# Optimization experiments

Hardware: AMD Instinct MI355X
Metric: run time of the kernel (lower is better)

Reference implementation:

```python
import jax, jax.numpy as jnp
import numpy as np

N_TOKENS = 16384
DIM = 2048
HIDDEN = 1408
N_EXPERTS = 8


def setup_inputs() -> dict:
    key = jax.random.key(0)
    k_x, k_w1, k_w2, k_w3 = jax.random.split(key, 4)
    x = jax.random.normal(k_x, (N_TOKENS, DIM), dtype=jnp.float32)
    # trunc_normal(std=0.02) approximated by scaled normal
    w1 = jax.random.normal(k_w1, (N_EXPERTS, HIDDEN, DIM), dtype=jnp.float32) * 0.02
    w2 = jax.random.normal(k_w2, (N_EXPERTS, DIM, HIDDEN), dtype=jnp.float32) * 0.02
    w3 = jax.random.normal(k_w3, (N_EXPERTS, HIDDEN, DIM), dtype=jnp.float32) * 0.02
    # contiguous, even token split across experts (sums to N_TOKENS)
    num_tokens_per_expert = jnp.full((N_EXPERTS,), N_TOKENS // N_EXPERTS, dtype=jnp.int32)
    return {"x": x, "w1": w1, "w2": w2, "w3": w3,
            "num_tokens_per_expert": num_tokens_per_expert}


def reference(x, w1, w2, w3, num_tokens_per_expert):
    """Masked per-expert SwiGLU FFN (matches _run_experts_for_loop).

    x: [N, D] tokens sorted so expert e owns the contiguous slice
       [cumsum_shifted[e], cumsum[e]).
    """
    n_tokens = x.shape[0]
    n_experts = w1.shape[0]
    cumsum = jnp.cumsum(num_tokens_per_expert.astype(jnp.int32))
    cumsum_shifted = jnp.concatenate(
        [jnp.zeros((1,), dtype=cumsum.dtype), cumsum[:-1]])
    token_idx = jnp.arange(n_tokens)
    out = jnp.zeros_like(x)
    for e in range(n_experts):  # small fixed expert loop, unrolled under jit
        mask = ((token_idx >= cumsum_shifted[e]) & (token_idx < cumsum[e]))
        mask = mask.astype(x.dtype)[:, None]          # [N, 1]
        x_masked = x * mask                            # [N, D]
        h = jax.nn.silu(x_masked @ w1[e].T)            # [N, H]
        h = h * (x_masked @ w3[e].T)                   # [N, H]
        out = out + (h @ w2[e].T) * mask               # [N, D]
    return out
```

## Files before the change

### kernel.cpp

```cpp
#include <hip/hip_runtime.h>
#include <stdint.h>

#define NTOK 16384
#define DIM 2048
#define HIDDEN 1408
#define NEXP 8
#define NPRIME 2816

typedef short short8 __attribute__((ext_vector_type(8)));
typedef float f32x4 __attribute__((ext_vector_type(4)));
typedef unsigned short u16;

__device__ __forceinline__ u16 f2bf(float f) {
    uint32_t u = __float_as_uint(f);
    return (u16)((u + 0x7fffu + ((u >> 16) & 1u)) >> 16);
}

__device__ __forceinline__ void gload16(const u16* g, u16* l) {
    __builtin_amdgcn_global_load_lds(
        (const __attribute__((address_space(1))) void*)g,
        (__attribute__((address_space(3))) void*)l,
        16, 0, 0);
}

__device__ __forceinline__ void stageA(const u16* Ag, size_t lda, int k2, u16* dst, int tid) {
    #pragma unroll
    for (int it = 0; it < 4; ++it) {
        int c   = it * 512 + tid;
        int row = c >> 3;
        int sc  = ((c & 7) ^ (row & 7)) << 3;
        gload16(Ag + (size_t)row * lda + k2 + sc, dst + c * 16 / 2);
    }
}
__device__ __forceinline__ void stageB(const u16* Bg, size_t ldb, int k2, u16* dst, int tid) {
    #pragma unroll
    for (int it = 0; it < 2; ++it) {
        int c   = it * 512 + tid;
        int row = c >> 3;
        int sc  = ((c & 7) ^ (row & 7)) << 3;
        gload16(Bg + (size_t)row * ldb + k2 + sc, dst + c * 8);
    }
}

__global__ __launch_bounds__(256) void cvt_kernel(const float* __restrict__ src,
                                                  u16* __restrict__ dst, long n) {
    long i0 = ((long)blockIdx.x * 256 + threadIdx.x) * 8;
    long stride = (long)gridDim.x * 256 * 8;
    for (long i = i0; i < n; i += stride) {
        float4 a = *(const float4*)(src + i);
        float4 b = *(const float4*)(src + i + 4);
        uint4 o;
        o.x = (uint32_t)f2bf(a.x) | ((uint32_t)f2bf(a.y) << 16);
        o.y = (uint32_t)f2bf(a.z) | ((uint32_t)f2bf(a.w) << 16);
        o.z = (uint32_t)f2bf(b.x) | ((uint32_t)f2bf(b.y) << 16);
        o.w = (uint32_t)f2bf(b.z) | ((uint32_t)f2bf(b.w) << 16);
        *(uint4*)(dst + i) = o;
    }
}

__global__ __launch_bounds__(256) void cvt13_kernel(const float* __restrict__ w1,
                                                    const float* __restrict__ w3,
                                                    u16* __restrict__ dst) {
    const int r  = blockIdx.x;
    const int e  = r / NPRIME;
    const int np = r - e * NPRIME;
    const int p  = np >> 5;
    const int s  = (np >> 4) & 1;
    const int c  = np & 15;
    const int hcol = p * 16 + c;
    const float* src = (s ? w3 : w1) + ((size_t)e * HIDDEN + hcol) * DIM;
    u16* d = dst + (size_t)r * DIM;
    const int i = threadIdx.x * 8;
    float4 a = *(const float4*)(src + i);
    float4 b = *(const float4*)(src + i + 4);
    uint4 o;
    o.x = (uint32_t)f2bf(a.x) | ((uint32_t)f2bf(a.y) << 16);
    o.y = (uint32_t)f2bf(a.z) | ((uint32_t)f2bf(a.w) << 16);
    o.z = (uint32_t)f2bf(b.x) | ((uint32_t)f2bf(b.y) << 16);
    o.w = (uint32_t)f2bf(b.z) | ((uint32_t)f2bf(b.w) << 16);
    *(uint4*)(d + i) = o;
}


#define GEMM_CORE(LD, NT, ACC_DECL)                                              \
    const int tid  = threadIdx.x;                                                \
    const int lane = tid & 63;                                                   \
    const int wid  = tid >> 6;                                                   \
    const int wr   = wid >> 1;                         \
    const int wc   = wid & 1;                          \
    const int lq   = lane >> 4;                                                  \
    const int lm   = lane & 15;                                                  \
    ACC_DECL;                                                                    \
    stageA(Ag, LD, 0,  As[0], tid);  stageB(Bg, LD, 0,  Bs[0], tid);             \
    stageA(Ag, LD, 64, As[1], tid);  stageB(Bg, LD, 64, Bs[1], tid);             \
    asm volatile("s_waitcnt vmcnt(6)" ::: "memory");                             \
    __builtin_amdgcn_s_barrier();                                                \
    for (int t = 0; t < NT; ++t) {                                               \
        const int p = t % 3, q = (t + 2) % 3;                                    \
        const u16* Asp = As[p];                                                  \
        const u16* Bsp = Bs[p];                                                  \
        short8 af0[2][2], af1[2][2], bf[4][2];                                   \
        _Pragma("unroll")                                                        \
        for (int i = 0; i < 2; ++i)                                              \
            _Pragma("unroll")                                                    \
            for (int kk = 0; kk < 2; ++kk) {                                     \
                int ar = wr * 64 + i * 16 + lm;                                  \
                int gc = kk * 4 + lq;                                            \
                af0[i][kk] = *(const short8*)&Asp[ar * 64 + ((gc ^ (ar & 7)) << 3)]; \
            }                                                                    \
        _Pragma("unroll")                                                        \
        for (int j = 0; j < 4; ++j)                                              \
            _Pragma("unroll")                                                    \
            for (int kk = 0; kk < 2; ++kk) {                                     \
                int br = wc * 64 + j * 16 + lm;                                  \
                int gc = kk * 4 + lq;                                            \
                bf[j][kk] = *(const short8*)&Bsp[br * 64 + ((gc ^ (br & 7)) << 3)]; \
            }                                                                    \
        if (t + 2 < NT) stageA(Ag, LD, (t + 2) * 64, As[q], tid);                \
        __builtin_amdgcn_s_barrier();                                            \
        __builtin_amdgcn_s_setprio(1);                                           \
        _Pragma("unroll")                                                        \
        for (int kk = 0; kk < 2; ++kk)                                           \
            _Pragma("unroll")                                                    \
            for (int i = 0; i < 2; ++i)                                          \
                _Pragma("unroll")                                                \
                for (int j = 0; j < 4; ++j)                                      \
                    acc[i][j] = __builtin_amdgcn_mfma_f32_16x16x32_bf16(         \
                        af0[i][kk], bf[j][kk], acc[i][j], 0, 0, 0);              \
        __builtin_amdgcn_s_setprio(0);                                           \
        __builtin_amdgcn_s_barrier();                                            \
        _Pragma("unroll")                                                        \
        for (int i = 0; i < 2; ++i)                                              \
            _Pragma("unroll")                                                    \
            for (int kk = 0; kk < 2; ++kk) {                                     \
                int ar = wr * 64 + (i + 2) * 16 + lm;                            \
                int gc = kk * 4 + lq;                                            \
                af1[i][kk] = *(const short8*)&Asp[ar * 64 + ((gc ^ (ar & 7)) << 3)]; \
            }                                                                    \
        if (t + 2 < NT) stageB(Bg, LD, (t + 2) * 64, Bs[q], tid);                \
        __builtin_amdgcn_s_barrier();                                            \
        __builtin_amdgcn_s_setprio(1);                                           \
        _Pragma("unroll")                                                        \
        for (int kk = 0; kk < 2; ++kk)                                           \
            _Pragma("unroll")                                                    \
            for (int i = 0; i < 2; ++i)                                          \
                _Pragma("unroll")                                                \
                for (int j = 0; j < 4; ++j)                                      \
                    acc[i + 2][j] = __builtin_amdgcn_mfma_f32_16x16x32_bf16(     \
                        af1[i][kk], bf[j][kk], acc[i + 2][j], 0, 0, 0);          \
        __builtin_amdgcn_s_setprio(0);                                           \
        if (t + 2 < NT) { asm volatile("s_waitcnt vmcnt(6)" ::: "memory"); }     \
        else            { asm volatile("s_waitcnt vmcnt(0)" ::: "memory"); }     \
        __builtin_amdgcn_s_barrier();                                            \
    }

__global__ __launch_bounds__(512, 1) void ffn1_kernel(
    const u16* __restrict__ xb, const u16* __restrict__ wb13,
    const int* __restrict__ ntpe, u16* __restrict__ hb)
{
    __shared__ u16 As[3][256 * 64];
    __shared__ u16 Bs[3][128 * 64];

    const int nwg = 8 * 22 * NEXP;
    int logical = (blockIdx.x & 7) * (nwg >> 3) + (blockIdx.x >> 3);
    const int mt = logical & 7;
    int rest = logical >> 3;
    const int nt = rest % 22;
    const int e  = rest / 22;

    int base = 0;
    #pragma unroll
    for (int i = 0; i < NEXP; ++i) base += (i < e) ? ntpe[i] : 0;
    const int cnt = ntpe[e];
    if (mt * 256 >= cnt) return;

    const size_t m0 = (size_t)base + (size_t)mt * 256;
    const u16* Ag = xb   + m0 * DIM;
    const u16* Bg = wb13 + ((size_t)e * NPRIME + nt * 128) * DIM;

    GEMM_CORE(DIM, 32, f32x4 acc[4][4] = {})

    #pragma unroll
    for (int i = 0; i < 4; ++i)
        #pragma unroll
        for (int jp = 0; jp < 4; jp += 2) {
            const int p = nt * 4 + wc * 2 + (jp >> 1);
            #pragma unroll
            for (int r = 0; r < 4; ++r) {
                int mrow = mt * 256 + wr * 64 + i * 16 + lq * 4 + r;
                if (mrow < cnt) {
                    float v1 = acc[i][jp][r];
                    float v3 = acc[i][jp + 1][r];
                    float h = (v1 / (1.f + __expf(-v1))) * v3;
                    hb[((size_t)base + mrow) * HIDDEN + p * 16 + lm] = f2bf(h);
                }
            }
        }
}

__global__ __launch_bounds__(512, 1) void ffn2_kernel(
    const u16* __restrict__ hb, const u16* __restrict__ w2b,
    const int* __restrict__ ntpe, float* __restrict__ out)
{
    __shared__ u16 As[3][256 * 64];
    __shared__ u16 Bs[3][128 * 64];

    const int nwg = 8 * 16 * NEXP;
    int logical = (blockIdx.x & 7) * (nwg >> 3) + (blockIdx.x >> 3);
    const int mt = logical & 7;
    int rest = logical >> 3;
    const int nt = rest % 16;
    const int e  = rest / 16;

    int base = 0;
    #pragma unroll
    for (int i = 0; i < NEXP; ++i) base += (i < e) ? ntpe[i] : 0;
    const int cnt = ntpe[e];
    if (mt * 256 >= cnt) return;

    const size_t m0 = (size_t)base + (size_t)mt * 256;
    const u16* Ag = hb  + m0 * HIDDEN;
    const u16* Bg = w2b + ((size_t)e * DIM + nt * 128) * HIDDEN;

    GEMM_CORE(HIDDEN, 22, f32x4 acc[4][4] = {})

    #pragma unroll
    for (int i = 0; i < 4; ++i)
        #pragma unroll
        for (int j = 0; j < 4; ++j)
            #pragma unroll
            for (int r = 0; r < 4; ++r) {
                int mrow = mt * 256 + wr * 64 + i * 16 + lq * 4 + r;
                if (mrow < cnt)
                    out[((size_t)base + mrow) * DIM + (nt * 128 + wc * 64 + j * 16 + lm)] = acc[i][j][r];
            }
}

extern "C" void kernel_launch(void* const* d_in, const int* in_sizes, int n_in,
                              void* d_out, int out_size, void* d_ws, size_t ws_size,
                              hipStream_t stream) {
    const float* x  = (const float*)d_in[0];
    const float* w1 = (const float*)d_in[1];
    const float* w2 = (const float*)d_in[2];
    const float* w3 = (const float*)d_in[3];
    const int* ntpe = (const int*)d_in[4];
    float* out = (float*)d_out;

    u16* xb   = (u16*)d_ws;
    u16* wb13 = xb   + (size_t)NTOK * DIM;
    u16* w2b  = wb13 + (size_t)NEXP * NPRIME * DIM;
    u16* hb   = w2b  + (size_t)NEXP * DIM * HIDDEN;

    cvt_kernel<<<2048, 256, 0, stream>>>(x,  xb,  (long)NTOK * DIM);
    cvt_kernel<<<2048, 256, 0, stream>>>(w2, w2b, (long)NEXP * DIM * HIDDEN);
    cvt13_kernel<<<NEXP * NPRIME, 256, 0, stream>>>(w1, w3, wb13);

    ffn1_kernel<<<8 * 22 * NEXP, 512, 0, stream>>>(xb, wb13, ntpe, hb);
    ffn2_kernel<<<8 * 16 * NEXP, 512, 0, stream>>>(hb, w2b, ntpe, out);
}
```

Baseline: 508.6 us.

## Enlarge GEMM tiles to 256x256 with two-stage half-tile staging

Both FFN GEMMs move from 256x128 output tiles with a three-stage LDS ring to 256x256 tiles with a double-buffered LDS layout. Each K-step is split into four phases, and each phase issues loads for one half of the next A or B tile. The wave grid becomes 2x4 with 8x4 accumulators per wave, which roughly halves the workgroup count and raises operand reuse per LDS load. The costs are a larger register footprint, a shallower prefetch pipeline and coarser tail waves, and the launch bounds now request two blocks per CU.

```diff
diff --git a/kernel.cpp b/kernel.cpp
--- a/kernel.cpp
+++ b/kernel.cpp
@@ -23,22 +23,26 @@
         16, 0, 0);
 }
 
-__device__ __forceinline__ void stageA(const u16* Ag, size_t lda, int k2, u16* dst, int tid) {
-    #pragma unroll
-    for (int it = 0; it < 4; ++it) {
-        int c   = it * 512 + tid;
-        int row = c >> 3;
-        int sc  = ((c & 7) ^ (row & 7)) << 3;
-        gload16(Ag + (size_t)row * lda + k2 + sc, dst + c * 16 / 2);
-    }
-}
-__device__ __forceinline__ void stageB(const u16* Bg, size_t ldb, int k2, u16* dst, int tid) {
+__device__ __forceinline__ void stage_half_A(const u16* Ag, size_t ld, int k2,
+                                             int h, u16* Abuf, int tid) {
     #pragma unroll
     for (int it = 0; it < 2; ++it) {
         int c   = it * 512 + tid;
-        int row = c >> 3;
-        int sc  = ((c & 7) ^ (row & 7)) << 3;
-        gload16(Bg + (size_t)row * ldb + k2 + sc, dst + c * 8);
+        int q   = (c >> 3) & 63;
+        int row = ((c >> 9) & 1) * 128 + h * 64 + q;
+        int sc  = ((c & 7) ^ (q & 7)) << 3;
+        gload16(Ag + (size_t)row * ld + k2 + sc, Abuf + h * 8192 + c * 8);
+    }
+}
+__device__ __forceinline__ void stage_half_B(const u16* Bg, size_t ld, int k2,
+                                             int h, u16* Bbuf, int tid) {
+    #pragma unroll
+    for (int it = 0; it < 2; ++it) {
+        int c   = it * 512 + tid;
+        int r   = c >> 3;
+        int row = h * 128 + r;
+        int sc  = ((c & 7) ^ (r & 7)) << 3;
+        gload16(Bg + (size_t)row * ld + k2 + sc, Bbuf + h * 8192 + c * 8);
     }
 }
 
@@ -82,91 +86,91 @@
 }
 
 
-#define GEMM_CORE(LD, NT, ACC_DECL)                                              \
-    const int tid  = threadIdx.x;                                                \
-    const int lane = tid & 63;                                                   \
-    const int wid  = tid >> 6;                                                   \
-    const int wr   = wid >> 1;                         \
-    const int wc   = wid & 1;                          \
-    const int lq   = lane >> 4;                                                  \
-    const int lm   = lane & 15;                                                  \
-    ACC_DECL;                                                                    \
-    stageA(Ag, LD, 0,  As[0], tid);  stageB(Bg, LD, 0,  Bs[0], tid);             \
-    stageA(Ag, LD, 64, As[1], tid);  stageB(Bg, LD, 64, Bs[1], tid);             \
-    asm volatile("s_waitcnt vmcnt(6)" ::: "memory");                             \
-    __builtin_amdgcn_s_barrier();                                                \
-    for (int t = 0; t < NT; ++t) {                                               \
-        const int p = t % 3, q = (t + 2) % 3;                                    \
-        const u16* Asp = As[p];                                                  \
-        const u16* Bsp = Bs[p];                                                  \
-        short8 af0[2][2], af1[2][2], bf[4][2];                                   \
-        _Pragma("unroll")                                                        \
-        for (int i = 0; i < 2; ++i)                                              \
-            _Pragma("unroll")                                                    \
-            for (int kk = 0; kk < 2; ++kk) {                                     \
-                int ar = wr * 64 + i * 16 + lm;                                  \
-                int gc = kk * 4 + lq;                                            \
-                af0[i][kk] = *(const short8*)&Asp[ar * 64 + ((gc ^ (ar & 7)) << 3)]; \
-            }                                                                    \
-        _Pragma("unroll")                                                        \
-        for (int j = 0; j < 4; ++j)                                              \
-            _Pragma("unroll")                                                    \
-            for (int kk = 0; kk < 2; ++kk) {                                     \
-                int br = wc * 64 + j * 16 + lm;                                  \
-                int gc = kk * 4 + lq;                                            \
-                bf[j][kk] = *(const short8*)&Bsp[br * 64 + ((gc ^ (br & 7)) << 3)]; \
-            }                                                                    \
-        if (t + 2 < NT) stageA(Ag, LD, (t + 2) * 64, As[q], tid);                \
-        __builtin_amdgcn_s_barrier();                                            \
-        __builtin_amdgcn_s_setprio(1);                                           \
-        _Pragma("unroll")                                                        \
-        for (int kk = 0; kk < 2; ++kk)                                           \
-            _Pragma("unroll")                                                    \
-            for (int i = 0; i < 2; ++i)                                          \
-                _Pragma("unroll")                                                \
-                for (int j = 0; j < 4; ++j)                                      \
-                    acc[i][j] = __builtin_amdgcn_mfma_f32_16x16x32_bf16(         \
-                        af0[i][kk], bf[j][kk], acc[i][j], 0, 0, 0);              \
-        __builtin_amdgcn_s_setprio(0);                                           \
-        __builtin_amdgcn_s_barrier();                                            \
-        _Pragma("unroll")                                                        \
-        for (int i = 0; i < 2; ++i)                                              \
-            _Pragma("unroll")                                                    \
-            for (int kk = 0; kk < 2; ++kk) {                                     \
-                int ar = wr * 64 + (i + 2) * 16 + lm;                            \
-                int gc = kk * 4 + lq;                                            \
-                af1[i][kk] = *(const short8*)&Asp[ar * 64 + ((gc ^ (ar & 7)) << 3)]; \
-            }                                                                    \
-        if (t + 2 < NT) stageB(Bg, LD, (t + 2) * 64, Bs[q], tid);                \
-        __builtin_amdgcn_s_barrier();                                            \
-        __builtin_amdgcn_s_setprio(1);                                           \
-        _Pragma("unroll")                                                        \
-        for (int kk = 0; kk < 2; ++kk)                                           \
-            _Pragma("unroll")                                                    \
-            for (int i = 0; i < 2; ++i)                                          \
-                _Pragma("unroll")                                                \
-                for (int j = 0; j < 4; ++j)                                      \
-                    acc[i + 2][j] = __builtin_amdgcn_mfma_f32_16x16x32_bf16(     \
-                        af1[i][kk], bf[j][kk], acc[i + 2][j], 0, 0, 0);          \
-        __builtin_amdgcn_s_setprio(0);                                           \
-        if (t + 2 < NT) { asm volatile("s_waitcnt vmcnt(6)" ::: "memory"); }     \
-        else            { asm volatile("s_waitcnt vmcnt(0)" ::: "memory"); }     \
-        __builtin_amdgcn_s_barrier();                                            \
-    }
-
-__global__ __launch_bounds__(512, 1) void ffn1_kernel(
+#define PHASE_TAIL(MH, BK_REGS)                                                 \
+    __builtin_amdgcn_s_barrier();                                               \
+    asm volatile("s_waitcnt lgkmcnt(0)" ::: "memory");                          \
+    __builtin_amdgcn_s_setprio(1);                                              \
+    _Pragma("unroll")                                                           \
+    for (int ii = 0; ii < 4; ++ii)                                              \
+        _Pragma("unroll")                                                       \
+        for (int j = 0; j < 4; ++j)                                             \
+            acc[MH * 4 + ii][j] = __builtin_amdgcn_mfma_f32_16x16x32_bf16(      \
+                af[ii], BK_REGS[j], acc[MH * 4 + ii][j], 0, 0, 0);              \
+    __builtin_amdgcn_s_setprio(0);
+
+#define GCORE(LD, NT)                                                           \
+    const int tid  = threadIdx.x;                                               \
+    const int lane = tid & 63;                                                  \
+    const int wid  = tid >> 6;                                                  \
+    const int wr   = wid >> 2;                       \
+    const int wc   = wid & 3;                        \
+    const int lq   = lane >> 4;                                                 \
+    const int lm   = lane & 15;                                                 \
+    const int xk   = lm & 7;                                                    \
+    f32x4 acc[8][4] = {};                                                       \
+    stage_half_A(Ag, LD, 0, 0, As[0], tid);                                     \
+    stage_half_B(Bg, LD, 0, 0, Bs[0], tid);                                     \
+    stage_half_A(Ag, LD, 0, 1, As[0], tid);                                     \
+    stage_half_B(Bg, LD, 0, 1, Bs[0], tid);                                     \
+    stage_half_A(Ag, LD, 64, 0, As[1], tid);                                    \
+    stage_half_B(Bg, LD, 64, 0, Bs[1], tid);                                    \
+    asm volatile("s_waitcnt vmcnt(4)" ::: "memory");                            \
+    __builtin_amdgcn_s_barrier();                                               \
+    for (int t = 0; t < NT; ++t) {                                              \
+        const u16* Ap = As[t & 1];                                              \
+        const u16* Bp = Bs[t & 1];                                              \
+        short8 af[4], bk0[4], bk1[4];                                           \
+                                                                   \
+        _Pragma("unroll")                                                       \
+        for (int ii = 0; ii < 4; ++ii)                                          \
+            af[ii] = *(const short8*)&Ap[(wr * 64 + ii * 16 + lm) * 64 + ((lq ^ xk) << 3)]; \
+        _Pragma("unroll")                                                       \
+        for (int j = 0; j < 4; ++j)                                             \
+            bk0[j] = *(const short8*)&Bp[(wc * 64 + j * 16 + lm) * 64 + ((lq ^ xk) << 3)]; \
+        if (t + 1 < NT) stage_half_A(Ag, LD, (t + 1) * 64, 1, As[(t + 1) & 1], tid); \
+        PHASE_TAIL(0, bk0)                                                      \
+        __builtin_amdgcn_s_barrier();                                           \
+                                                                   \
+        _Pragma("unroll")                                                       \
+        for (int ii = 0; ii < 4; ++ii)                                          \
+            af[ii] = *(const short8*)&Ap[(wr * 64 + ii * 16 + lm) * 64 + (((4 + lq) ^ xk) << 3)]; \
+        _Pragma("unroll")                                                       \
+        for (int j = 0; j < 4; ++j)                                             \
+            bk1[j] = *(const short8*)&Bp[(wc * 64 + j * 16 + lm) * 64 + (((4 + lq) ^ xk) << 3)]; \
+        if (t + 1 < NT) stage_half_B(Bg, LD, (t + 1) * 64, 1, Bs[(t + 1) & 1], tid); \
+        PHASE_TAIL(0, bk1)                                                      \
+        __builtin_amdgcn_s_barrier();                                           \
+                                                                   \
+        _Pragma("unroll")                                                       \
+        for (int ii = 0; ii < 4; ++ii)                                          \
+            af[ii] = *(const short8*)&Ap[(128 + wr * 64 + ii * 16 + lm) * 64 + ((lq ^ xk) << 3)]; \
+        if (t + 2 < NT) stage_half_A(Ag, LD, (t + 2) * 64, 0, As[t & 1], tid);  \
+        PHASE_TAIL(1, bk0)                                                      \
+        __builtin_amdgcn_s_barrier();                                           \
+                                                                   \
+        _Pragma("unroll")                                                       \
+        for (int ii = 0; ii < 4; ++ii)                                          \
+            af[ii] = *(const short8*)&Ap[(128 + wr * 64 + ii * 16 + lm) * 64 + (((4 + lq) ^ xk) << 3)]; \
+        if (t + 2 < NT) stage_half_B(Bg, LD, (t + 2) * 64, 0, Bs[t & 1], tid);  \
+        PHASE_TAIL(1, bk1)                                                      \
+        if (t + 2 < NT) { asm volatile("s_waitcnt vmcnt(4)" ::: "memory"); }    \
+        else            { asm volatile("s_waitcnt vmcnt(0)" ::: "memory"); }    \
+        __builtin_amdgcn_s_barrier();                                           \
+    }
+
+__global__ __launch_bounds__(512, 2) void ffn1_kernel(
     const u16* __restrict__ xb, const u16* __restrict__ wb13,
     const int* __restrict__ ntpe, u16* __restrict__ hb)
 {
-    __shared__ u16 As[3][256 * 64];
-    __shared__ u16 Bs[3][128 * 64];
-
-    const int nwg = 8 * 22 * NEXP;
+    __shared__ __align__(16) u16 As[2][16384];
+    __shared__ __align__(16) u16 Bs[2][16384];
+
+    const int nwg = 8 * 11 * NEXP;
     int logical = (blockIdx.x & 7) * (nwg >> 3) + (blockIdx.x >> 3);
     const int mt = logical & 7;
     int rest = logical >> 3;
-    const int nt = rest % 22;
-    const int e  = rest / 22;
+    const int nt = rest % 11;
+    const int e  = rest / 11;
 
     int base = 0;
     #pragma unroll
@@ -176,41 +180,41 @@
 
     const size_t m0 = (size_t)base + (size_t)mt * 256;
     const u16* Ag = xb   + m0 * DIM;
-    const u16* Bg = wb13 + ((size_t)e * NPRIME + nt * 128) * DIM;
-
-    GEMM_CORE(DIM, 32, f32x4 acc[4][4] = {})
-
-    #pragma unroll
-    for (int i = 0; i < 4; ++i)
+    const u16* Bg = wb13 + ((size_t)e * NPRIME + nt * 256) * DIM;
+
+    GCORE(DIM, 32)
+
+    #pragma unroll
+    for (int i = 0; i < 8; ++i)
         #pragma unroll
         for (int jp = 0; jp < 4; jp += 2) {
-            const int p = nt * 4 + wc * 2 + (jp >> 1);
+            const int p16 = nt * 8 + wc * 2 + (jp >> 1);
             #pragma unroll
             for (int r = 0; r < 4; ++r) {
-                int mrow = mt * 256 + wr * 64 + i * 16 + lq * 4 + r;
+                int mrow = mt * 256 + wr * 128 + i * 16 + lq * 4 + r;
                 if (mrow < cnt) {
                     float v1 = acc[i][jp][r];
                     float v3 = acc[i][jp + 1][r];
                     float h = (v1 / (1.f + __expf(-v1))) * v3;
-                    hb[((size_t)base + mrow) * HIDDEN + p * 16 + lm] = f2bf(h);
+                    hb[((size_t)base + mrow) * HIDDEN + p16 * 16 + lm] = f2bf(h);
                 }
             }
         }
 }
 
-__global__ __launch_bounds__(512, 1) void ffn2_kernel(
+__global__ __launch_bounds__(512, 2) void ffn2_kernel(
     const u16* __restrict__ hb, const u16* __restrict__ w2b,
     const int* __restrict__ ntpe, float* __restrict__ out)
 {
-    __shared__ u16 As[3][256 * 64];
-    __shared__ u16 Bs[3][128 * 64];
-
-    const int nwg = 8 * 16 * NEXP;
+    __shared__ __align__(16) u16 As[2][16384];
+    __shared__ __align__(16) u16 Bs[2][16384];
+
+    const int nwg = 8 * 8 * NEXP;
     int logical = (blockIdx.x & 7) * (nwg >> 3) + (blockIdx.x >> 3);
     const int mt = logical & 7;
     int rest = logical >> 3;
-    const int nt = rest % 16;
-    const int e  = rest / 16;
+    const int nt = rest % 8;
+    const int e  = rest / 8;
 
     int base = 0;
     #pragma unroll
@@ -220,19 +224,19 @@
 
     const size_t m0 = (size_t)base + (size_t)mt * 256;
     const u16* Ag = hb  + m0 * HIDDEN;
-    const u16* Bg = w2b + ((size_t)e * DIM + nt * 128) * HIDDEN;
-
-    GEMM_CORE(HIDDEN, 22, f32x4 acc[4][4] = {})
-
-    #pragma unroll
-    for (int i = 0; i < 4; ++i)
+    const u16* Bg = w2b + ((size_t)e * DIM + nt * 256) * HIDDEN;
+
+    GCORE(HIDDEN, 22)
+
+    #pragma unroll
+    for (int i = 0; i < 8; ++i)
         #pragma unroll
         for (int j = 0; j < 4; ++j)
             #pragma unroll
             for (int r = 0; r < 4; ++r) {
-                int mrow = mt * 256 + wr * 64 + i * 16 + lq * 4 + r;
+                int mrow = mt * 256 + wr * 128 + i * 16 + lq * 4 + r;
                 if (mrow < cnt)
-                    out[((size_t)base + mrow) * DIM + (nt * 128 + wc * 64 + j * 16 + lm)] = acc[i][j][r];
+                    out[((size_t)base + mrow) * DIM + (nt * 256 + wc * 64 + j * 16 + lm)] = acc[i][j][r];
             }
 }
 
@@ -255,6 +259,6 @@
     cvt_kernel<<<2048, 256, 0, stream>>>(w2, w2b, (long)NEXP * DIM * HIDDEN);
     cvt13_kernel<<<NEXP * NPRIME, 256, 0, stream>>>(w1, w3, wb13);
 
-    ffn1_kernel<<<8 * 22 * NEXP, 512, 0, stream>>>(xb, wb13, ntpe, hb);
-    ffn2_kernel<<<8 * 16 * NEXP, 512, 0, stream>>>(hb, w2b, ntpe, out);
-}
+    ffn1_kernel<<<8 * 11 * NEXP, 512, 0, stream>>>(xb, wb13, ntpe, hb);
+    ffn2_kernel<<<8 * 8 * NEXP, 512, 0, stream>>>(hb, w2b, ntpe, out);
+}
```

Result: slower. 546.0 us (+7.3%).
